# Kernel optimization log

Measured on AMD Instinct MI355X. Metric: run time of the kernel, lower is better.

## Reference

```python
import jax, jax.numpy as jnp
import numpy as np

B, S, D = 2, 2048, 1024
H = 16
DK = D // H


def setup_inputs() -> dict:
    key = jax.random.key(0)
    ks = jax.random.split(key, 5)
    std = np.sqrt(2.0 / (D + D))
    x = jax.random.normal(ks[0], (B, S, D), dtype=jnp.float32)
    wq = jax.random.normal(ks[1], (D, D), dtype=jnp.float32) * std
    wk = jax.random.normal(ks[2], (D, D), dtype=jnp.float32) * std
    wv = jax.random.normal(ks[3], (D, D), dtype=jnp.float32) * std
    wo = jax.random.normal(ks[4], (D, D), dtype=jnp.float32) * std
    return {"x": x, "wq": wq, "wk": wk, "wv": wv, "wo": wo}


def reference(x, wq, wk, wv, wo):
    # Linear: y = x @ W.T  (weight stored as [d_out, d_in])
    q = jnp.einsum("bsd,ed->bse", x, wq)
    k = jnp.einsum("bsd,ed->bse", x, wk)
    v = jnp.einsum("bsd,ed->bse", x, wv)
    # split heads: [B, S, H*DK] -> [B, H, S, DK]
    q = q.reshape(B, S, H, DK).transpose(0, 2, 1, 3)
    k = k.reshape(B, S, H, DK).transpose(0, 2, 1, 3)
    v = v.reshape(B, S, H, DK).transpose(0, 2, 1, 3)
    scale = 1.0 / jnp.sqrt(jnp.asarray(DK, dtype=x.dtype))
    scores = jnp.einsum("bhqd,bhkd->bhqk", q, k) * scale  # [B,H,S,S]
    causal = jnp.tril(jnp.ones((S, S), dtype=bool))
    scores = jnp.where(causal, scores, -jnp.inf)
    attn = jax.nn.softmax(scores, axis=-1)
    out = jnp.einsum("bhqk,bhkd->bhqd", attn, v)  # [B,H,S,DK]
    out = out.transpose(0, 2, 1, 3).reshape(B, S, D)
    return jnp.einsum("bsd,ed->bse", out, wo)
```

## Files before the change

kernel.cpp:

```cpp
#include <hip/hip_runtime.h>
#include <hip/hip_bf16.h>
#include <cstdint>

#define B_ 2
#define S_ 2048
#define D_ 1024
#define H_ 16
#define DK_ 64

typedef __attribute__((ext_vector_type(8))) short bf16x8;
typedef __attribute__((ext_vector_type(4))) float f32x4;

__device__ __forceinline__ unsigned short f2bf(float f) {
  unsigned u = __float_as_uint(f);
  u = (u + 0x7FFFu + ((u >> 16) & 1u)) >> 16;
  return (unsigned short)u;
}

typedef __attribute__((address_space(1))) void gv_t;
typedef __attribute__((address_space(3))) void lv_t;
__device__ __forceinline__ void gl16(const void* g, void* l) {
  __builtin_amdgcn_global_load_lds((gv_t*)g, (lv_t*)l, 16, 0, 0);
}

__device__ __forceinline__ void stage8w(const unsigned short* gbase, size_t ldg,
                                        unsigned short* lds, int wave, int lane) {
  const int lr = lane >> 3;
  const int col8 = (lane & 7) ^ lr;
  gl16(gbase + (size_t)(wave * 8 + lr) * ldg + col8 * 8, lds + wave * 512);
}

__device__ __forceinline__ bf16x8 rdswz(const unsigned short* lds, int row, int col) {
  return *(const bf16x8*)&lds[row * 64 + (col ^ ((row & 7) << 3))];
}

__global__ void cvt_kernel(const float* __restrict__ in, unsigned short* __restrict__ out, int n4) {
  int i = blockIdx.x * blockDim.x + threadIdx.x;
  if (i >= n4) return;
  const float4 v = reinterpret_cast<const float4*>(in)[i];
  ushort4 o;
  o.x = f2bf(v.x); o.y = f2bf(v.y); o.z = f2bf(v.z); o.w = f2bf(v.w);
  reinterpret_cast<ushort4*>(out)[i] = o;
}

__global__ void cvtw_kernel(const float* __restrict__ w0, const float* __restrict__ w1,
                            const float* __restrict__ w2, const float* __restrict__ w3,
                            unsigned short* __restrict__ o0, unsigned short* __restrict__ o1,
                            unsigned short* __restrict__ o2, unsigned short* __restrict__ o3) {
  const int mat = blockIdx.y;
  const float* in = (mat == 0) ? w0 : (mat == 1) ? w1 : (mat == 2) ? w2 : w3;
  unsigned short* out = (mat == 0) ? o0 : (mat == 1) ? o1 : (mat == 2) ? o2 : o3;
  int i = blockIdx.x * blockDim.x + threadIdx.x;
  const float4 v = reinterpret_cast<const float4*>(in)[i];
  ushort4 o;
  o.x = f2bf(v.x); o.y = f2bf(v.y); o.z = f2bf(v.z); o.w = f2bf(v.w);
  reinterpret_cast<ushort4*>(out)[i] = o;
}

#define BM 128
#define BK 64

template <typename OutT, bool TV2, int BNv>
__global__ __launch_bounds__(256) void gemm_bt(
    const unsigned short* __restrict__ A,
    const unsigned short* __restrict__ B0, const unsigned short* __restrict__ B1,
    const unsigned short* __restrict__ B2,
    OutT* __restrict__ C0, OutT* __restrict__ C1, OutT* __restrict__ C2,
    int M, int N, int K) {
  constexpr int NFRAG = BNv / 32;
  __shared__ unsigned short lA[BM * BK];
  __shared__ unsigned short lB[BNv * BK];
  const int tid = threadIdx.x;
  const int wave = tid >> 6, lane = tid & 63;
  const int l16 = lane & 15, lqq = lane >> 4;
  const int wr = wave >> 1, wc = wave & 1;
  const int lr = lane >> 3;
  const int col8 = ((lane & 7) ^ lr) * 8;

  const int tilesPerMat = N / BNv;
  const int bx = blockIdx.x;
  const int mat = bx / tilesPerMat;
  const int n0 = (bx % tilesPerMat) * BNv;
  const unsigned short* Bm = (mat == 0) ? B0 : (mat == 1) ? B1 : B2;
  OutT* C = (mat == 0) ? C0 : (mat == 1) ? C1 : C2;
  const int m0 = blockIdx.y * BM;

  f32x4 acc[4][NFRAG] = {};

  for (int k0 = 0; k0 < K; k0 += BK) {
    __syncthreads();
#pragma unroll
    for (int c = wave; c < 16; c += 4)
      gl16(A + (size_t)(m0 + c * 8 + lr) * K + k0 + col8, &lA[c * 512]);
#pragma unroll
    for (int c = wave; c < BNv / 8; c += 4)
      gl16(Bm + (size_t)(n0 + c * 8 + lr) * K + k0 + col8, &lB[c * 512]);
    __syncthreads();
#pragma unroll
    for (int kk = 0; kk < BK / 32; ++kk) {
      bf16x8 af[4], bfr[NFRAG];
#pragma unroll
      for (int m = 0; m < 4; ++m)
        af[m] = rdswz(lA, wr * 64 + m * 16 + l16, kk * 32 + lqq * 8);
#pragma unroll
      for (int n = 0; n < NFRAG; ++n)
        bfr[n] = rdswz(lB, wc * (BNv / 2) + n * 16 + l16, kk * 32 + lqq * 8);
      __builtin_amdgcn_s_setprio(1);
#pragma unroll
      for (int m = 0; m < 4; ++m)
#pragma unroll
        for (int n = 0; n < NFRAG; ++n)
          acc[m][n] = __builtin_amdgcn_mfma_f32_16x16x32_bf16(af[m], bfr[n], acc[m][n], 0, 0, 0);
      __builtin_amdgcn_s_setprio(0);
    }
  }

  if (TV2 && mat == 2) {
    unsigned short* Vt = (unsigned short*)C;
#pragma unroll
    for (int m = 0; m < 4; ++m)
#pragma unroll
      for (int n = 0; n < NFRAG; ++n) {
        int r0 = m0 + wr * 64 + m * 16 + lqq * 4;
        int cidx = n0 + wc * (BNv / 2) + n * 16 + l16;
        int bb = r0 >> 11, s = r0 & 2047;
        int h = cidx >> 6, dv = cidx & 63;
        ushort4 o;
        o.x = f2bf(acc[m][n][0]); o.y = f2bf(acc[m][n][1]);
        o.z = f2bf(acc[m][n][2]); o.w = f2bf(acc[m][n][3]);
        *(ushort4*)(Vt + ((size_t)((bb * H_ + h) * DK_ + dv)) * S_ + s) = o;
      }
  } else {
#pragma unroll
    for (int m = 0; m < 4; ++m)
#pragma unroll
      for (int n = 0; n < NFRAG; ++n)
#pragma unroll
        for (int j = 0; j < 4; ++j) {
          int r = m0 + wr * 64 + m * 16 + lqq * 4 + j;
          int cidx = n0 + wc * (BNv / 2) + n * 16 + l16;
          float v = acc[m][n][j];
          if constexpr (sizeof(OutT) == 4) C[(size_t)r * N + cidx] = v;
          else C[(size_t)r * N + cidx] = f2bf(v);
        }
  }
}

__global__ __launch_bounds__(512) void attn_kernel(
    const unsigned short* __restrict__ Qg, const unsigned short* __restrict__ Kg,
    const unsigned short* __restrict__ Vtg, unsigned short* __restrict__ Og) {
  __shared__ unsigned short sQ[2][64 * 64];
  __shared__ unsigned short sK[2][64 * 64];
  __shared__ unsigned short sVt[2][64 * 64];
  __shared__ unsigned short sP[8][2][16 * 64];
  const int tid = threadIdx.x, wave = tid >> 6, lane = tid & 63;
  const int side = wave >> 2, wq = wave & 3;
  const int l16 = lane & 15, lq = lane >> 4;
  const int id = blockIdx.x;
  const int bh = (id & 7) * 4 + ((id >> 3) & 3);
  const int g = (id >> 5) & 7;
  const int i = (id < 256) ? (15 - g) : g;
  const int b = bh >> 4, h = bh & 15;
  const int qtA = 2 * i, qtB = 2 * i + 1;
  const int qt_s = side ? qtB : qtA;
  const int NT = i + 1;
  const size_t tokbase = (size_t)b * S_ * D_ + h * DK_;
  const unsigned short* VtB = Vtg + (size_t)(b * H_ + h) * DK_ * S_;
  unsigned short (*sPw)[16 * 64] = sP[wave];

  stage8w(Qg + tokbase + (size_t)(qtA * 64) * D_, D_, sQ[0], wave, lane);
  stage8w(Qg + tokbase + (size_t)(qtB * 64) * D_, D_, sQ[1], wave, lane);
  __syncthreads();
  bf16x8 aq0 = rdswz(sQ[side], wq * 16 + l16, lq * 8);
  bf16x8 aq1 = rdswz(sQ[side], wq * 16 + l16, 32 + lq * 8);

  const float LOG2E_S = 0.125f * 1.44269504f;
  const float THR2 = 11.5416f;
  float m_run[4] = {-1e30f, -1e30f, -1e30f, -1e30f};
  float l_run[4] = {0.f, 0.f, 0.f, 0.f};
  f32x4 o_acc[4] = {};

#pragma unroll 1
  for (int kt = 0; kt < NT; ++kt) {
    __syncthreads();
    stage8w(Kg + tokbase + (size_t)(kt * 128) * D_, D_, sK[0], wave, lane);
    stage8w(Kg + tokbase + (size_t)(kt * 128 + 64) * D_, D_, sK[1], wave, lane);
    stage8w(VtB + kt * 128, S_, sVt[0], wave, lane);
    stage8w(VtB + kt * 128 + 64, S_, sVt[1], wave, lane);
    __syncthreads();

    const bool last = (kt == NT - 1);
    float p[8][4];

#pragma unroll
    for (int sub = 0; sub < 2; ++sub) {
      const bool skip = (sub == 1) && (side == 0) && last;
      if (!skip) {
        __builtin_amdgcn_s_setprio(1);
#pragma unroll
        for (int nb = 0; nb < 4; ++nb) {
          bf16x8 bk0 = rdswz(sK[sub], nb * 16 + l16, lq * 8);
          bf16x8 bk1 = rdswz(sK[sub], nb * 16 + l16, 32 + lq * 8);
          f32x4 a = {};
          a = __builtin_amdgcn_mfma_f32_16x16x32_bf16(aq0, bk0, a, 0, 0, 0);
          a = __builtin_amdgcn_mfma_f32_16x16x32_bf16(aq1, bk1, a, 0, 0, 0);
#pragma unroll
          for (int j = 0; j < 4; ++j) p[sub * 4 + nb][j] = a[j] * LOG2E_S;
        }
        __builtin_amdgcn_s_setprio(0);
      } else {
#pragma unroll
        for (int nb = 0; nb < 4; ++nb)
#pragma unroll
          for (int j = 0; j < 4; ++j) p[sub * 4 + nb][j] = -1e30f;
      }
    }

    if (last) {
      if (side == 0) {
#pragma unroll
        for (int nb = 0; nb < 4; ++nb)
#pragma unroll
          for (int j = 0; j < 4; ++j) {
            int kidx = nb * 16 + l16;
            int qidx = wq * 16 + lq * 4 + j;
            if (kidx > qidx) p[nb][j] = -1e30f;
          }
      } else {
#pragma unroll
        for (int nb = 0; nb < 4; ++nb)
#pragma unroll
          for (int j = 0; j < 4; ++j) {
            int kidx = nb * 16 + l16;
            int qidx = wq * 16 + lq * 4 + j;
            if (kidx > qidx) p[4 + nb][j] = -1e30f;
          }
      }
    }

    float pmax[4];
    bool ok = true;
#pragma unroll
    for (int j = 0; j < 4; ++j) {
      float r = p[0][j];
#pragma unroll
      for (int nbb = 1; nbb < 8; ++nbb) r = fmaxf(r, p[nbb][j]);
      pmax[j] = r;
      ok = ok && (r <= m_run[j] + THR2);
    }
    if (!__all((int)ok)) {
#pragma unroll
      for (int j = 0; j < 4; ++j) {
        float r = pmax[j];
#pragma unroll
        for (int d = 1; d < 16; d <<= 1) r = fmaxf(r, __shfl_xor(r, d));
        float mn = fmaxf(m_run[j], r);
        float alpha = exp2f(m_run[j] - mn);
        m_run[j] = mn;
        l_run[j] *= alpha;
#pragma unroll
        for (int nb = 0; nb < 4; ++nb) o_acc[nb][j] *= alpha;
      }
    }
#pragma unroll
    for (int j = 0; j < 4; ++j) {
      const int rw = lq * 4 + j;
#pragma unroll
      for (int nbb = 0; nbb < 8; ++nbb) {
        float e = exp2f(p[nbb][j] - m_run[j]);
        l_run[j] += e;
        sPw[nbb >> 2][rw * 64 + (((nbb & 3) * 16 + l16) ^ ((rw & 7) << 3))] = f2bf(e);
      }
    }

    __builtin_amdgcn_s_setprio(1);
#pragma unroll
    for (int sub = 0; sub < 2; ++sub)
#pragma unroll
      for (int kk = 0; kk < 2; ++kk) {
        bf16x8 ap = rdswz(sPw[sub], l16, kk * 32 + lq * 8);
#pragma unroll
        for (int nb = 0; nb < 4; ++nb) {
          bf16x8 bv = rdswz(sVt[sub], nb * 16 + l16, kk * 32 + lq * 8);
          o_acc[nb] = __builtin_amdgcn_mfma_f32_16x16x32_bf16(ap, bv, o_acc[nb], 0, 0, 0);
        }
      }
    __builtin_amdgcn_s_setprio(0);
  }

#pragma unroll
  for (int j = 0; j < 4; ++j) {
    float s = l_run[j];
#pragma unroll
    for (int d = 1; d < 16; d <<= 1) s += __shfl_xor(s, d);
    float inv = 1.f / s;
#pragma unroll
    for (int nb = 0; nb < 4; ++nb) {
      int r = qt_s * 64 + wq * 16 + lq * 4 + j;
      Og[tokbase + (size_t)r * D_ + nb * 16 + l16] = f2bf(o_acc[nb][j] * inv);
    }
  }
}

extern "C" void kernel_launch(void* const* d_in, const int* in_sizes, int n_in,
                              void* d_out, int out_size, void* d_ws, size_t ws_size,
                              hipStream_t stream) {
  const float* x = (const float*)d_in[0];
  const float* wq = (const float*)d_in[1];
  const float* wk = (const float*)d_in[2];
  const float* wv = (const float*)d_in[3];
  const float* wo = (const float*)d_in[4];
  float* out = (float*)d_out;

  char* ws = (char*)d_ws;
  const size_t MB = 1024 * 1024;
  unsigned short* xb  = (unsigned short*)(ws + 0);
  unsigned short* wqb = (unsigned short*)(ws + 8 * MB);
  unsigned short* wkb = (unsigned short*)(ws + 10 * MB);
  unsigned short* wvb = (unsigned short*)(ws + 12 * MB);
  unsigned short* wob = (unsigned short*)(ws + 14 * MB);
  unsigned short* Qb  = (unsigned short*)(ws + 16 * MB);
  unsigned short* Kb  = (unsigned short*)(ws + 24 * MB);
  unsigned short* Vtb = (unsigned short*)(ws + 32 * MB);
  unsigned short* AOb = (unsigned short*)(ws + 40 * MB);

  const int M = B_ * S_;
  const int N = D_, K = D_;

  cvt_kernel<<<dim3((M * D_ / 4 + 255) / 256), 256, 0, stream>>>(x, xb, M * D_ / 4);
  cvtw_kernel<<<dim3(D_ * D_ / 4 / 256, 4), 256, 0, stream>>>(wq, wk, wv, wo, wqb, wkb, wvb, wob);

  gemm_bt<unsigned short, true, 128><<<dim3(3 * (N / 128), M / BM), 256, 0, stream>>>(
      xb, wqb, wkb, wvb, Qb, Kb, Vtb, M, N, K);

  attn_kernel<<<dim3(512), 512, 0, stream>>>(Qb, Kb, Vtb, AOb);

  gemm_bt<float, false, 64><<<dim3(N / 64, M / BM), 256, 0, stream>>>(
      AOb, wob, wob, wob, out, out, out, M, N, K);
}
```

Before: 121.0 us.

## Fold softmax scale into Q projection, MFMA row sums, merge convert kernels

The log2e/sqrt(dk) score scale is applied in the Q projection epilogue, which removes a per-score multiply from the attention loop. Softmax row sums are now accumulated by an extra MFMA against a ones vector, replacing the VALU adds and the final shuffle reduction. The P store uses the hardware bf16 conversion. The x and weight conversions are merged into one launch. The extra MFMAs add matrix-unit work, and the 5-row grid launches many idle blocks for the small weight matrices.

```diff
diff --git a/kernel.cpp b/kernel.cpp
--- a/kernel.cpp
+++ b/kernel.cpp
@@ -8,6 +8,8 @@
 #define H_ 16
 #define DK_ 64
 
+#define LOG2E_S 0.18033688f
+
 typedef __attribute__((ext_vector_type(8))) short bf16x8;
 typedef __attribute__((ext_vector_type(4))) float f32x4;
 
@@ -15,6 +17,11 @@
   unsigned u = __float_as_uint(f);
   u = (u + 0x7FFFu + ((u >> 16) & 1u)) >> 16;
   return (unsigned short)u;
+}
+
+__device__ __forceinline__ unsigned short f2bf_hw(float f) {
+  __hip_bfloat16 h = __float2bfloat16(f);
+  return *reinterpret_cast<unsigned short*>(&h);
 }
 
 typedef __attribute__((address_space(1))) void gv_t;
@@ -34,7 +41,16 @@
   return *(const bf16x8*)&lds[row * 64 + (col ^ ((row & 7) << 3))];
 }
 
-__global__ void cvt_kernel(const float* __restrict__ in, unsigned short* __restrict__ out, int n4) {
+__global__ void cvt_all_kernel(const float* __restrict__ x,
+                               const float* __restrict__ w0, const float* __restrict__ w1,
+                               const float* __restrict__ w2, const float* __restrict__ w3,
+                               unsigned short* __restrict__ xo,
+                               unsigned short* __restrict__ o0, unsigned short* __restrict__ o1,
+                               unsigned short* __restrict__ o2, unsigned short* __restrict__ o3) {
+  const int mat = blockIdx.y;
+  const float* in = (mat == 0) ? x : (mat == 1) ? w0 : (mat == 2) ? w1 : (mat == 3) ? w2 : w3;
+  unsigned short* out = (mat == 0) ? xo : (mat == 1) ? o0 : (mat == 2) ? o1 : (mat == 3) ? o2 : o3;
+  const int n4 = (mat == 0) ? (B_ * S_ * D_ / 4) : (D_ * D_ / 4);
   int i = blockIdx.x * blockDim.x + threadIdx.x;
   if (i >= n4) return;
   const float4 v = reinterpret_cast<const float4*>(in)[i];
@@ -43,24 +59,10 @@
   reinterpret_cast<ushort4*>(out)[i] = o;
 }
 
-__global__ void cvtw_kernel(const float* __restrict__ w0, const float* __restrict__ w1,
-                            const float* __restrict__ w2, const float* __restrict__ w3,
-                            unsigned short* __restrict__ o0, unsigned short* __restrict__ o1,
-                            unsigned short* __restrict__ o2, unsigned short* __restrict__ o3) {
-  const int mat = blockIdx.y;
-  const float* in = (mat == 0) ? w0 : (mat == 1) ? w1 : (mat == 2) ? w2 : w3;
-  unsigned short* out = (mat == 0) ? o0 : (mat == 1) ? o1 : (mat == 2) ? o2 : o3;
-  int i = blockIdx.x * blockDim.x + threadIdx.x;
-  const float4 v = reinterpret_cast<const float4*>(in)[i];
-  ushort4 o;
-  o.x = f2bf(v.x); o.y = f2bf(v.y); o.z = f2bf(v.z); o.w = f2bf(v.w);
-  reinterpret_cast<ushort4*>(out)[i] = o;
-}
-
 #define BM 128
 #define BK 64
 
-template <typename OutT, bool TV2, int BNv>
+template <typename OutT, bool TV2, int BNv, bool SCALEQ>
 __global__ __launch_bounds__(256) void gemm_bt(
     const unsigned short* __restrict__ A,
     const unsigned short* __restrict__ B0, const unsigned short* __restrict__ B1,
@@ -131,6 +133,7 @@
         *(ushort4*)(Vt + ((size_t)((bb * H_ + h) * DK_ + dv)) * S_ + s) = o;
       }
   } else {
+    const float cscale = (SCALEQ && mat == 0) ? LOG2E_S : 1.0f;
 #pragma unroll
     for (int m = 0; m < 4; ++m)
 #pragma unroll
@@ -139,7 +142,7 @@
         for (int j = 0; j < 4; ++j) {
           int r = m0 + wr * 64 + m * 16 + lqq * 4 + j;
           int cidx = n0 + wc * (BNv / 2) + n * 16 + l16;
-          float v = acc[m][n][j];
+          float v = acc[m][n][j] * cscale;
           if constexpr (sizeof(OutT) == 4) C[(size_t)r * N + cidx] = v;
           else C[(size_t)r * N + cidx] = f2bf(v);
         }
@@ -174,10 +177,11 @@
   bf16x8 aq0 = rdswz(sQ[side], wq * 16 + l16, lq * 8);
   bf16x8 aq1 = rdswz(sQ[side], wq * 16 + l16, 32 + lq * 8);
 
-  const float LOG2E_S = 0.125f * 1.44269504f;
   const float THR2 = 11.5416f;
+  const short ONE_BF = 0x3F80;
+  const bf16x8 vones = {ONE_BF, ONE_BF, ONE_BF, ONE_BF, ONE_BF, ONE_BF, ONE_BF, ONE_BF};
   float m_run[4] = {-1e30f, -1e30f, -1e30f, -1e30f};
-  float l_run[4] = {0.f, 0.f, 0.f, 0.f};
+  f32x4 sum_acc = {};
   f32x4 o_acc[4] = {};
 
 #pragma unroll 1
@@ -205,7 +209,7 @@
           a = __builtin_amdgcn_mfma_f32_16x16x32_bf16(aq0, bk0, a, 0, 0, 0);
           a = __builtin_amdgcn_mfma_f32_16x16x32_bf16(aq1, bk1, a, 0, 0, 0);
 #pragma unroll
-          for (int j = 0; j < 4; ++j) p[sub * 4 + nb][j] = a[j] * LOG2E_S;
+          for (int j = 0; j < 4; ++j) p[sub * 4 + nb][j] = a[j];
         }
         __builtin_amdgcn_s_setprio(0);
       } else {
@@ -257,7 +261,7 @@
         float mn = fmaxf(m_run[j], r);
         float alpha = exp2f(m_run[j] - mn);
         m_run[j] = mn;
-        l_run[j] *= alpha;
+        sum_acc[j] *= alpha;
 #pragma unroll
         for (int nb = 0; nb < 4; ++nb) o_acc[nb][j] *= alpha;
       }
@@ -268,8 +272,7 @@
 #pragma unroll
       for (int nbb = 0; nbb < 8; ++nbb) {
         float e = exp2f(p[nbb][j] - m_run[j]);
-        l_run[j] += e;
-        sPw[nbb >> 2][rw * 64 + (((nbb & 3) * 16 + l16) ^ ((rw & 7) << 3))] = f2bf(e);
+        sPw[nbb >> 2][rw * 64 + (((nbb & 3) * 16 + l16) ^ ((rw & 7) << 3))] = f2bf_hw(e);
       }
     }
 
@@ -279,6 +282,7 @@
 #pragma unroll
       for (int kk = 0; kk < 2; ++kk) {
         bf16x8 ap = rdswz(sPw[sub], l16, kk * 32 + lq * 8);
+        sum_acc = __builtin_amdgcn_mfma_f32_16x16x32_bf16(ap, vones, sum_acc, 0, 0, 0);
 #pragma unroll
         for (int nb = 0; nb < 4; ++nb) {
           bf16x8 bv = rdswz(sVt[sub], nb * 16 + l16, kk * 32 + lq * 8);
@@ -290,10 +294,7 @@
 
 #pragma unroll
   for (int j = 0; j < 4; ++j) {
-    float s = l_run[j];
-#pragma unroll
-    for (int d = 1; d < 16; d <<= 1) s += __shfl_xor(s, d);
-    float inv = 1.f / s;
+    float inv = 1.f / sum_acc[j];
 #pragma unroll
     for (int nb = 0; nb < 4; ++nb) {
       int r = qt_s * 64 + wq * 16 + lq * 4 + j;
@@ -327,14 +328,14 @@
   const int M = B_ * S_;
   const int N = D_, K = D_;
 
-  cvt_kernel<<<dim3((M * D_ / 4 + 255) / 256), 256, 0, stream>>>(x, xb, M * D_ / 4);
-  cvtw_kernel<<<dim3(D_ * D_ / 4 / 256, 4), 256, 0, stream>>>(wq, wk, wv, wo, wqb, wkb, wvb, wob);
-
-  gemm_bt<unsigned short, true, 128><<<dim3(3 * (N / 128), M / BM), 256, 0, stream>>>(
+  cvt_all_kernel<<<dim3(B_ * S_ * D_ / 4 / 256, 5), 256, 0, stream>>>(
+      x, wq, wk, wv, wo, xb, wqb, wkb, wvb, wob);
+
+  gemm_bt<unsigned short, true, 128, true><<<dim3(3 * (N / 128), M / BM), 256, 0, stream>>>(
       xb, wqb, wkb, wvb, Qb, Kb, Vtb, M, N, K);
 
   attn_kernel<<<dim3(512), 512, 0, stream>>>(Qb, Kb, Vtb, AOb);
 
-  gemm_bt<float, false, 64><<<dim3(N / 64, M / BM), 256, 0, stream>>>(
+  gemm_bt<float, false, 64, false><<<dim3(N / 64, M / BM), 256, 0, stream>>>(
       AOb, wob, wob, wob, out, out, out, M, N, K);
 }
```

Result: faster. 111.2 us (-8.1%).
